# Performance work log

Hardware: AMD Instinct MI355X
Metric: run time of the kernel (lower is better)

The kernel has to match this reference:

```python
import jax, jax.numpy as jnp
import numpy as np

B, T, C, H = 4, 2048, 1024, 16
D = C // H  # head dim = 64

def setup_inputs() -> dict:
    key = jax.random.key(0)
    k1, k2, k3 = jax.random.split(key, 3)
    x = jax.random.normal(k1, (B, T, C), dtype=jnp.float32)
    w_attn = jax.random.normal(k2, (C, 3 * C), dtype=jnp.float32) * 0.02
    b_attn = jnp.zeros((3 * C,), dtype=jnp.float32)
    w_proj = jax.random.normal(k3, (C, C), dtype=jnp.float32) * 0.02
    b_proj = jnp.zeros((C,), dtype=jnp.float32)
    return {"x": x, "w_attn": w_attn, "b_attn": b_attn, "w_proj": w_proj, "b_proj": b_proj}

def reference(x, w_attn, b_attn, w_proj, b_proj):
    Bx, Tx, Cx = x.shape
    qkv = x @ w_attn + b_attn  # [B, T, 3C]
    q, k, v = jnp.split(qkv, 3, axis=2)
    # [B, H, T, D]
    q = q.reshape(Bx, Tx, H, D).swapaxes(1, 2)
    k = k.reshape(Bx, Tx, H, D).swapaxes(1, 2)
    v = v.reshape(Bx, Tx, H, D).swapaxes(1, 2)
    scale = 1.0 / jnp.sqrt(jnp.asarray(D, dtype=x.dtype))
    att = jnp.einsum('bhqd,bhkd->bhqk', q, k) * scale  # [B, H, T, T]
    causal = jnp.tril(jnp.ones((Tx, Tx), dtype=bool))
    att = jnp.where(causal[None, None], att, -jnp.inf)
    att = jax.nn.softmax(att, axis=-1)
    y = jnp.einsum('bhqk,bhkd->bhqd', att, v)  # [B, H, T, D]
    y = y.swapaxes(1, 2).reshape(Bx, Tx, Cx)
    return y @ w_proj + b_proj
```

## Files before the change

kernel.cpp:

```cpp
#include <hip/hip_runtime.h>
#include <hip/hip_bf16.h>
#include <cstdint>

#define B_ 4
#define T_ 2048
#define C_ 1024
#define H_ 16
#define D_ 64

typedef __bf16 bf16x8 __attribute__((ext_vector_type(8)));
typedef float f32x4 __attribute__((ext_vector_type(4)));

static __device__ __forceinline__ float bf2f(unsigned short u) {
    union { unsigned int i; float f; } w;
    w.i = ((unsigned int)u) << 16;
    return w.f;
}
static __device__ __forceinline__ unsigned short f2bf(float f) {
    unsigned int i = __float_as_uint(f);
    unsigned int r = (i + 0x7FFFu + ((i >> 16) & 1u)) >> 16;
    return (unsigned short)r;
}
static __device__ __forceinline__ float exp2_fast(float x) {
    float r;
    asm("v_exp_f32 %0, %1" : "=v"(r) : "v"(x));
    return r;
}

static __device__ __forceinline__ void gl_lds16(const unsigned short* g,
                                                unsigned short* l) {
    __builtin_amdgcn_global_load_lds(
        (const __attribute__((address_space(1))) unsigned int*)g,
        (__attribute__((address_space(3))) unsigned int*)l, 16, 0, 0);
}

__global__ __launch_bounds__(256)
void convert_f32_bf16(const float* __restrict__ in,
                      unsigned short* __restrict__ out, int n) {
    int i = (blockIdx.x * 256 + threadIdx.x) * 8;
    if (i < n) {
        float4 a = *(const float4*)(in + i);
        float4 b = *(const float4*)(in + i + 4);
        ushort4 s0 = {f2bf(a.x), f2bf(a.y), f2bf(a.z), f2bf(a.w)};
        ushort4 s1 = {f2bf(b.x), f2bf(b.y), f2bf(b.z), f2bf(b.w)};
        *(ushort4*)(out + i) = s0;
        *(ushort4*)(out + i + 4) = s1;
    }
}

__global__ void transpose_f32_bf16(const float* __restrict__ in,
                                   unsigned short* __restrict__ out,
                                   int R, int Cc) {
    __shared__ unsigned short tile[32][33];
    int c0 = blockIdx.x * 32;
    int r0 = blockIdx.y * 32;
    int tx = threadIdx.x, ty = threadIdx.y;
    #pragma unroll
    for (int i = ty; i < 32; i += 8)
        tile[i][tx] = f2bf(in[(size_t)(r0 + i) * Cc + c0 + tx]);
    __syncthreads();
    #pragma unroll
    for (int i = ty; i < 32; i += 8)
        out[(size_t)(c0 + i) * R + r0 + tx] = tile[tx][i];
}

__global__ void transpose_v(const unsigned short* __restrict__ qkv,
                            unsigned short* __restrict__ vt) {
    __shared__ unsigned short tile[32][33];
    int bh = blockIdx.z;
    int b = bh >> 4, h = bh & 15;
    int t0 = blockIdx.x * 32;
    int d0 = blockIdx.y * 32;
    int tx = threadIdx.x, ty = threadIdx.y;
    const unsigned short* src = qkv + (size_t)b * T_ * 3 * C_ + 2 * C_ + h * 64;
    #pragma unroll
    for (int i = ty; i < 32; i += 8)
        tile[i][tx] = src[(size_t)(t0 + i) * 3 * C_ + d0 + tx];
    __syncthreads();
    unsigned short* dst = vt + (size_t)bh * 64 * T_;
    #pragma unroll
    for (int i = ty; i < 32; i += 8)
        dst[(size_t)(d0 + i) * T_ + t0 + tx] = tile[tx][i];
}

template <bool OUT_F32>
__global__ __launch_bounds__(256)
void gemm_bt(const unsigned short* __restrict__ A, int lda,
             const unsigned short* __restrict__ Bt,
             const float* __restrict__ bias,
             void* __restrict__ Cptr,
             int M, int N, int K, float qscale, int qcols) {
    __shared__ __align__(16) unsigned short As[128][32];
    __shared__ __align__(16) unsigned short Bs[128][32];

    int tid = threadIdx.x;
    int row0 = blockIdx.y * 128;
    int col0 = blockIdx.x * 128;
    int wave = tid >> 6;
    int lane = tid & 63;
    int wm = wave >> 1, wn = wave & 1;
    int m16 = lane & 15, quad = lane >> 4;

    f32x4 acc[4][4];
    #pragma unroll
    for (int i = 0; i < 4; ++i)
        #pragma unroll
        for (int j = 0; j < 4; ++j)
            acc[i][j] = (f32x4){0.f, 0.f, 0.f, 0.f};

    for (int k0 = 0; k0 < K; k0 += 32) {
        #pragma unroll
        for (int it = 0; it < 2; ++it) {
            int c = tid + it * 256;
            int r = c >> 2, ko = (c & 3) << 3;
            gl_lds16(A + (size_t)(row0 + r) * lda + k0 + ko, &As[0][0] + (size_t)c * 8);
            gl_lds16(Bt + (size_t)(col0 + r) * K + k0 + ko, &Bs[0][0] + (size_t)c * 8);
        }
        __syncthreads();

        bf16x8 af[4], bfr[4];
        #pragma unroll
        for (int i = 0; i < 4; ++i)
            af[i] = *(const bf16x8*)&As[wm * 64 + i * 16 + m16][quad * 8];
        #pragma unroll
        for (int j = 0; j < 4; ++j)
            bfr[j] = *(const bf16x8*)&Bs[wn * 64 + j * 16 + m16][quad * 8];
        #pragma unroll
        for (int i = 0; i < 4; ++i)
            #pragma unroll
            for (int j = 0; j < 4; ++j)
                acc[i][j] = __builtin_amdgcn_mfma_f32_16x16x32_bf16(
                    af[i], bfr[j], acc[i][j], 0, 0, 0);
        __syncthreads();
    }

    #pragma unroll
    for (int j = 0; j < 4; ++j) {
        int col = col0 + wn * 64 + j * 16 + m16;
        float bv = bias[col];
        float sc = (col < qcols) ? qscale : 1.0f;
        #pragma unroll
        for (int i = 0; i < 4; ++i) {
            int row = row0 + wm * 64 + i * 16 + quad * 4;
            #pragma unroll
            for (int rr = 0; rr < 4; ++rr) {
                float v = (acc[i][j][rr] + bv) * sc;
                if constexpr (OUT_F32)
                    ((float*)Cptr)[(size_t)(row + rr) * N + col] = v;
                else
                    ((unsigned short*)Cptr)[(size_t)(row + rr) * N + col] = f2bf(v);
            }
        }
    }
}

__global__ __launch_bounds__(256)
void attn_mfma(unsigned short* __restrict__ qkv,
               const unsigned short* __restrict__ vt) {
    __shared__ __align__(16) unsigned short Ks[2][64][80];
    __shared__ __align__(16) unsigned short Vs[2][64][80];
    __shared__ __align__(16) unsigned short Pb[4][16][72];

    int bh = blockIdx.x;
    int b = bh >> 4, h = bh & 15;
    int qb = (T_ / 64 - 1) - blockIdx.y;
    int tid = threadIdx.x;
    int wave = tid >> 6;
    int lane = tid & 63;
    int m16 = lane & 15, quad = lane >> 4;

    const size_t rs = 3 * C_;
    unsigned short* base = qkv + (size_t)b * T_ * rs + h * 64;
    const unsigned short* kb0 = base + C_;
    const unsigned short* vtb = vt + (size_t)bh * 64 * T_;

    int qrow = qb * 64 + wave * 16 + m16;
    const unsigned short* qp = base + (size_t)qrow * rs;
    bf16x8 qf0 = *(const bf16x8*)(qp + quad * 8);
    bf16x8 qf1 = *(const bf16x8*)(qp + 32 + quad * 8);

    f32x4 o[4];
    #pragma unroll
    for (int dt = 0; dt < 4; ++dt) o[dt] = (f32x4){0.f, 0.f, 0.f, 0.f};
    float lrow[4] = {0.f, 0.f, 0.f, 0.f};

    int qg0 = qb * 64 + wave * 16 + quad * 4;
    int ntiles = qb + 1;

    int kkey = tid >> 3, kdc = (tid & 7) << 3;
    int vd   = tid >> 3, vkc = (tid & 7) << 3;

    uint4 ra  = *(const uint4*)(kb0 + (size_t)kkey * rs + kdc);
    uint4 rb  = *(const uint4*)(kb0 + (size_t)(kkey + 32) * rs + kdc);
    uint4 rva = *(const uint4*)(vtb + (size_t)vd * T_ + vkc);
    uint4 rvb = *(const uint4*)(vtb + (size_t)(vd + 32) * T_ + vkc);
    *(uint4*)&Ks[0][kkey][kdc]      = ra;
    *(uint4*)&Ks[0][kkey + 32][kdc] = rb;
    *(uint4*)&Vs[0][vd][vkc]        = rva;
    *(uint4*)&Vs[0][vd + 32][vkc]   = rvb;
    if (ntiles > 1) {
        const unsigned short* kn = kb0 + (size_t)64 * rs;
        ra  = *(const uint4*)(kn + (size_t)kkey * rs + kdc);
        rb  = *(const uint4*)(kn + (size_t)(kkey + 32) * rs + kdc);
        rva = *(const uint4*)(vtb + (size_t)vd * T_ + 64 + vkc);
        rvb = *(const uint4*)(vtb + (size_t)(vd + 32) * T_ + 64 + vkc);
    }
    __syncthreads();

    for (int kt = 0; kt < ntiles; ++kt) {
        int cur = kt & 1;

        f32x4 s[4];
        #pragma unroll
        for (int st = 0; st < 4; ++st) {
            f32x4 acc = (f32x4){0.f, 0.f, 0.f, 0.f};
            bf16x8 k0 = *(const bf16x8*)&Ks[cur][st * 16 + m16][quad * 8];
            bf16x8 k1 = *(const bf16x8*)&Ks[cur][st * 16 + m16][32 + quad * 8];
            acc = __builtin_amdgcn_mfma_f32_16x16x32_bf16(qf0, k0, acc, 0, 0, 0);
            acc = __builtin_amdgcn_mfma_f32_16x16x32_bf16(qf1, k1, acc, 0, 0, 0);
            s[st] = acc;
        }

        if (kt == qb) {
            #pragma unroll
            for (int st = 0; st < 4; ++st) {
                int kg = kt * 64 + st * 16 + m16;
                #pragma unroll
                for (int r = 0; r < 4; ++r)
                    if (kg > qg0 + r) s[st][r] = -1.0e30f;
            }
        }

        #pragma unroll
        for (int st = 0; st < 4; ++st) {
            #pragma unroll
            for (int r = 0; r < 4; ++r) {
                float p = exp2_fast(s[st][r]);
                lrow[r] += p;
                Pb[wave][quad * 4 + r][st * 16 + m16] = f2bf(p);
            }
        }
        __builtin_amdgcn_sched_barrier(0);

        #pragma unroll
        for (int s2 = 0; s2 < 2; ++s2) {
            bf16x8 pa = *(const bf16x8*)&Pb[wave][m16][s2 * 32 + quad * 8];
            #pragma unroll
            for (int dt = 0; dt < 4; ++dt) {
                bf16x8 vv = *(const bf16x8*)&Vs[cur][dt * 16 + m16][s2 * 32 + quad * 8];
                o[dt] = __builtin_amdgcn_mfma_f32_16x16x32_bf16(pa, vv, o[dt], 0, 0, 0);
            }
        }

        if (kt + 1 < ntiles) {
            int nxt = (kt + 1) & 1;
            *(uint4*)&Ks[nxt][kkey][kdc]      = ra;
            *(uint4*)&Ks[nxt][kkey + 32][kdc] = rb;
            *(uint4*)&Vs[nxt][vd][vkc]        = rva;
            *(uint4*)&Vs[nxt][vd + 32][vkc]   = rvb;
            if (kt + 2 < ntiles) {
                const unsigned short* kn = kb0 + (size_t)((kt + 2) * 64) * rs;
                ra  = *(const uint4*)(kn + (size_t)kkey * rs + kdc);
                rb  = *(const uint4*)(kn + (size_t)(kkey + 32) * rs + kdc);
                rva = *(const uint4*)(vtb + (size_t)vd * T_ + (kt + 2) * 64 + vkc);
                rvb = *(const uint4*)(vtb + (size_t)(vd + 32) * T_ + (kt + 2) * 64 + vkc);
            }
        }
        __syncthreads();
    }

    float lf[4];
    #pragma unroll
    for (int r = 0; r < 4; ++r) lf[r] = lrow[r];
    #pragma unroll
    for (int off = 1; off <= 8; off <<= 1)
        #pragma unroll
        for (int r = 0; r < 4; ++r)
            lf[r] += __shfl_xor(lf[r], off);

    #pragma unroll
    for (int r = 0; r < 4; ++r) {
        float inv = 1.0f / lf[r];
        unsigned short* op = base + (size_t)(qg0 + r) * rs;
        #pragma unroll
        for (int dt = 0; dt < 4; ++dt)
            op[dt * 16 + m16] = f2bf(o[dt][r] * inv);
    }
}

extern "C" void kernel_launch(void* const* d_in, const int* in_sizes, int n_in,
                              void* d_out, int out_size, void* d_ws, size_t ws_size,
                              hipStream_t stream) {
    const float* x      = (const float*)d_in[0];
    const float* w_attn = (const float*)d_in[1];
    const float* b_attn = (const float*)d_in[2];
    const float* w_proj = (const float*)d_in[3];
    const float* b_proj = (const float*)d_in[4];
    float* out = (float*)d_out;

    unsigned short* ws = (unsigned short*)d_ws;
    unsigned short* xb       = ws;
    unsigned short* w_attn_t = xb + (size_t)B_ * T_ * C_;
    unsigned short* w_proj_t = w_attn_t + (size_t)3 * C_ * C_;
    unsigned short* qkv      = w_proj_t + (size_t)C_ * C_;

    const size_t fixed_hw = (size_t)B_ * T_ * C_ + 4 * (size_t)C_ * C_;
    const size_t qkv_full = (size_t)B_ * T_ * 3 * C_;
    int bstep = (ws_size >= (fixed_hw + qkv_full) * sizeof(unsigned short)) ? B_ : 1;

    int nx = B_ * T_ * C_;
    convert_f32_bf16<<<nx / 2048, 256, 0, stream>>>(x, xb, nx);
    transpose_f32_bf16<<<dim3(3 * C_ / 32, C_ / 32), dim3(32, 8), 0, stream>>>(
        w_attn, w_attn_t, C_, 3 * C_);
    transpose_f32_bf16<<<dim3(C_ / 32, C_ / 32), dim3(32, 8), 0, stream>>>(
        w_proj, w_proj_t, C_, C_);

    const float QSCALE = 0.125f * 1.44269504088896341f;

    for (int b0 = 0; b0 < B_; b0 += bstep) {
        int M = bstep * T_;
        const unsigned short* xbb = xb + (size_t)b0 * T_ * C_;
        float* ob = out + (size_t)b0 * T_ * C_;
        unsigned short* vt = (bstep == B_)
            ? xb
            : qkv + (size_t)bstep * T_ * 3 * C_;

        gemm_bt<false><<<dim3(3 * C_ / 128, M / 128), 256, 0, stream>>>(
            xbb, C_, w_attn_t, b_attn, qkv, M, 3 * C_, C_, QSCALE, C_);

        transpose_v<<<dim3(T_ / 32, 2, bstep * H_), dim3(32, 8), 0, stream>>>(
            qkv, vt);

        attn_mfma<<<dim3(bstep * H_, T_ / 64), 256, 0, stream>>>(qkv, vt);

        gemm_bt<true><<<dim3(C_ / 128, M / 128), 256, 0, stream>>>(
            qkv, 3 * C_, w_proj_t, b_proj, ob, M, C_, C_, 1.0f, 0);
    }
}
```

Baseline: 282.9 us.

## Fuse V transpose into QKV GEMM epilogue and stage coalesced stores through LDS

The QKV GEMM epilogue now stages each wave's output sub-tiles through shared memory. Q and K go to a compact 2C-wide buffer with vectorized row stores, and V is written directly in transposed per-head layout. This removes the separate transpose_v kernel and its extra read/write of V. It also replaces the scattered 2-byte epilogue stores with 8-byte coalesced ones. The attention kernel's row stride drops to 2C, which shrinks its memory footprint, at the cost of a more complex epilogue with extra LDS traffic.

Result: faster. 272.7 us (-3.6%).

```diff
diff --git a/kernel.cpp b/kernel.cpp
--- a/kernel.cpp
+++ b/kernel.cpp
@@ -64,32 +64,14 @@
         out[(size_t)(c0 + i) * R + r0 + tx] = tile[tx][i];
 }
 
-__global__ void transpose_v(const unsigned short* __restrict__ qkv,
-                            unsigned short* __restrict__ vt) {
-    __shared__ unsigned short tile[32][33];
-    int bh = blockIdx.z;
-    int b = bh >> 4, h = bh & 15;
-    int t0 = blockIdx.x * 32;
-    int d0 = blockIdx.y * 32;
-    int tx = threadIdx.x, ty = threadIdx.y;
-    const unsigned short* src = qkv + (size_t)b * T_ * 3 * C_ + 2 * C_ + h * 64;
-    #pragma unroll
-    for (int i = ty; i < 32; i += 8)
-        tile[i][tx] = src[(size_t)(t0 + i) * 3 * C_ + d0 + tx];
-    __syncthreads();
-    unsigned short* dst = vt + (size_t)bh * 64 * T_;
-    #pragma unroll
-    for (int i = ty; i < 32; i += 8)
-        dst[(size_t)(d0 + i) * T_ + t0 + tx] = tile[tx][i];
-}
-
-template <bool OUT_F32>
 __global__ __launch_bounds__(256)
-void gemm_bt(const unsigned short* __restrict__ A, int lda,
-             const unsigned short* __restrict__ Bt,
-             const float* __restrict__ bias,
-             void* __restrict__ Cptr,
-             int M, int N, int K, float qscale, int qcols) {
+void gemm_qkv(const unsigned short* __restrict__ A,
+              const unsigned short* __restrict__ Bt,
+              const float* __restrict__ bias,
+              unsigned short* __restrict__ qkv,
+              unsigned short* __restrict__ vt,
+              int M, float qscale) {
+    const int N = 3 * C_, K = C_;
     __shared__ __align__(16) unsigned short As[128][32];
     __shared__ __align__(16) unsigned short Bs[128][32];
 
@@ -113,7 +95,7 @@
         for (int it = 0; it < 2; ++it) {
             int c = tid + it * 256;
             int r = c >> 2, ko = (c & 3) << 3;
-            gl_lds16(A + (size_t)(row0 + r) * lda + k0 + ko, &As[0][0] + (size_t)c * 8);
+            gl_lds16(A + (size_t)(row0 + r) * K + k0 + ko, &As[0][0] + (size_t)c * 8);
             gl_lds16(Bt + (size_t)(col0 + r) * K + k0 + ko, &Bs[0][0] + (size_t)c * 8);
         }
         __syncthreads();
@@ -134,22 +116,125 @@
         __syncthreads();
     }
 
+    float bv[4];
+    #pragma unroll
+    for (int j = 0; j < 4; ++j)
+        bv[j] = bias[col0 + wn * 64 + j * 16 + m16];
+
+    unsigned short* wbuf = &As[0][0] + wave * 2048;
+    bool isV = (col0 >= 2 * C_);
+    float sc = (col0 < C_) ? qscale : 1.0f;
+    int b_loc = row0 >> 11;
+    int trow0 = (row0 & 2047) + wm * 64;
+
+    #pragma unroll
+    for (int sub = 0; sub < 4; ++sub) {
+        int i0 = (sub >> 1) << 1;
+        int j0 = (sub & 1) << 1;
+        #pragma unroll
+        for (int jj = 0; jj < 2; ++jj) {
+            #pragma unroll
+            for (int ii = 0; ii < 2; ++ii) {
+                #pragma unroll
+                for (int rr = 0; rr < 4; ++rr) {
+                    int rl = ii * 16 + quad * 4 + rr;
+                    int cl = jj * 16 + m16;
+                    unsigned short hv =
+                        f2bf((acc[i0 + ii][j0 + jj][rr] + bv[j0 + jj]) * sc);
+                    if (!isV) wbuf[rl * 40 + cl] = hv;
+                    else      wbuf[cl * 40 + rl] = hv;
+                }
+            }
+        }
+        __builtin_amdgcn_sched_barrier(0);
+        if (!isV) {
+            #pragma unroll
+            for (int it = 0; it < 4; ++it) {
+                int rl = it * 8 + (lane >> 3);
+                int cc = (lane & 7) << 2;
+                uint2 v2 = *(const uint2*)&wbuf[rl * 40 + cc];
+                int rowg = row0 + wm * 64 + i0 * 16 + rl;
+                int colg = col0 + wn * 64 + j0 * 16 + cc;
+                *(uint2*)&qkv[(size_t)rowg * (2 * C_) + colg] = v2;
+            }
+        } else {
+            int head = ((col0 - 2 * C_) + wn * 64) >> 6;
+            unsigned short* vtb =
+                vt + (size_t)((b_loc * H_ + head) * 64) * T_;
+            #pragma unroll
+            for (int it = 0; it < 4; ++it) {
+                int dsub = it * 8 + (lane >> 3);
+                int tc = (lane & 7) << 2;
+                uint2 v2 = *(const uint2*)&wbuf[dsub * 40 + tc];
+                int d = j0 * 16 + dsub;
+                int tg = trow0 + i0 * 16 + tc;
+                *(uint2*)&vtb[(size_t)d * T_ + tg] = v2;
+            }
+        }
+        __builtin_amdgcn_sched_barrier(0);
+    }
+}
+
+__global__ __launch_bounds__(256)
+void gemm_out(const unsigned short* __restrict__ A, int lda,
+              const unsigned short* __restrict__ Bt,
+              const float* __restrict__ bias,
+              float* __restrict__ Cmat,
+              int M, int N, int K) {
+    __shared__ __align__(16) unsigned short As[128][32];
+    __shared__ __align__(16) unsigned short Bs[128][32];
+
+    int tid = threadIdx.x;
+    int row0 = blockIdx.y * 128;
+    int col0 = blockIdx.x * 128;
+    int wave = tid >> 6;
+    int lane = tid & 63;
+    int wm = wave >> 1, wn = wave & 1;
+    int m16 = lane & 15, quad = lane >> 4;
+
+    f32x4 acc[4][4];
+    #pragma unroll
+    for (int i = 0; i < 4; ++i)
+        #pragma unroll
+        for (int j = 0; j < 4; ++j)
+            acc[i][j] = (f32x4){0.f, 0.f, 0.f, 0.f};
+
+    for (int k0 = 0; k0 < K; k0 += 32) {
+        #pragma unroll
+        for (int it = 0; it < 2; ++it) {
+            int c = tid + it * 256;
+            int r = c >> 2, ko = (c & 3) << 3;
+            gl_lds16(A + (size_t)(row0 + r) * lda + k0 + ko, &As[0][0] + (size_t)c * 8);
+            gl_lds16(Bt + (size_t)(col0 + r) * K + k0 + ko, &Bs[0][0] + (size_t)c * 8);
+        }
+        __syncthreads();
+
+        bf16x8 af[4], bfr[4];
+        #pragma unroll
+        for (int i = 0; i < 4; ++i)
+            af[i] = *(const bf16x8*)&As[wm * 64 + i * 16 + m16][quad * 8];
+        #pragma unroll
+        for (int j = 0; j < 4; ++j)
+            bfr[j] = *(const bf16x8*)&Bs[wn * 64 + j * 16 + m16][quad * 8];
+        #pragma unroll
+        for (int i = 0; i < 4; ++i)
+            #pragma unroll
+            for (int j = 0; j < 4; ++j)
+                acc[i][j] = __builtin_amdgcn_mfma_f32_16x16x32_bf16(
+                    af[i], bfr[j], acc[i][j], 0, 0, 0);
+        __syncthreads();
+    }
+
     #pragma unroll
     for (int j = 0; j < 4; ++j) {
         int col = col0 + wn * 64 + j * 16 + m16;
-        float bv = bias[col];
-        float sc = (col < qcols) ? qscale : 1.0f;
+        float bvv = bias[col];
         #pragma unroll
         for (int i = 0; i < 4; ++i) {
             int row = row0 + wm * 64 + i * 16 + quad * 4;
             #pragma unroll
-            for (int rr = 0; rr < 4; ++rr) {
-                float v = (acc[i][j][rr] + bv) * sc;
-                if constexpr (OUT_F32)
-                    ((float*)Cptr)[(size_t)(row + rr) * N + col] = v;
-                else
-                    ((unsigned short*)Cptr)[(size_t)(row + rr) * N + col] = f2bf(v);
-            }
+            for (int rr = 0; rr < 4; ++rr)
+                Cmat[(size_t)(row + rr) * N + col] = acc[i][j][rr] + bvv;
         }
     }
 }
@@ -169,7 +254,7 @@
     int lane = tid & 63;
     int m16 = lane & 15, quad = lane >> 4;
 
-    const size_t rs = 3 * C_;
+    const size_t rs = 2 * C_;
     unsigned short* base = qkv + (size_t)b * T_ * rs + h * 64;
     const unsigned short* kb0 = base + C_;
     const unsigned short* vtb = vt + (size_t)bh * 64 * T_;
@@ -305,8 +390,9 @@
     unsigned short* qkv      = w_proj_t + (size_t)C_ * C_;
 
     const size_t fixed_hw = (size_t)B_ * T_ * C_ + 4 * (size_t)C_ * C_;
-    const size_t qkv_full = (size_t)B_ * T_ * 3 * C_;
-    int bstep = (ws_size >= (fixed_hw + qkv_full) * sizeof(unsigned short)) ? B_ : 1;
+    const size_t per_b_hw = (size_t)T_ * 2 * C_ + (size_t)H_ * 64 * T_;
+    int bstep = (ws_size >= (fixed_hw + (size_t)B_ * per_b_hw) * sizeof(unsigned short))
+                ? B_ : 1;
 
     int nx = B_ * T_ * C_;
     convert_f32_bf16<<<nx / 2048, 256, 0, stream>>>(x, xb, nx);
@@ -321,19 +407,14 @@
         int M = bstep * T_;
         const unsigned short* xbb = xb + (size_t)b0 * T_ * C_;
         float* ob = out + (size_t)b0 * T_ * C_;
-        unsigned short* vt = (bstep == B_)
-            ? xb
-            : qkv + (size_t)bstep * T_ * 3 * C_;
-
-        gemm_bt<false><<<dim3(3 * C_ / 128, M / 128), 256, 0, stream>>>(
-            xbb, C_, w_attn_t, b_attn, qkv, M, 3 * C_, C_, QSCALE, C_);
-
-        transpose_v<<<dim3(T_ / 32, 2, bstep * H_), dim3(32, 8), 0, stream>>>(
-            qkv, vt);
+        unsigned short* vt = qkv + (size_t)bstep * T_ * 2 * C_;
+
+        gemm_qkv<<<dim3(3 * C_ / 128, M / 128), 256, 0, stream>>>(
+            xbb, w_attn_t, b_attn, qkv, vt, M, QSCALE);
 
         attn_mfma<<<dim3(bstep * H_, T_ / 64), 256, 0, stream>>>(qkv, vt);
 
-        gemm_bt<true><<<dim3(C_ / 128, M / 128), 256, 0, stream>>>(
-            qkv, 3 * C_, w_proj_t, b_proj, ob, M, C_, C_, 1.0f, 0);
-    }
-}
+        gemm_out<<<dim3(C_ / 128, M / 128), 256, 0, stream>>>(
+            qkv, 2 * C_, w_proj_t, b_proj, ob, M, C_, C_);
+    }
+}
```
